# Performance work log

Hardware: AMD Instinct MI355X
Metric: run time of the kernel (lower is better)

The kernel has to match this reference:

```python
import jax, jax.numpy as jnp
import numpy as np

B, C_IN, C_OUT, N, E = 1, 64, 64, 100000, 3200000
BN_EPS = 1e-5


def setup_inputs() -> dict:
    key = jax.random.key(0)
    ks = jax.random.split(key, 8)
    return {
        "in_features": jax.random.normal(ks[0], (B, C_IN, N), dtype=jnp.float32),
        "w_v": jax.random.normal(ks[1], (C_OUT, C_IN), dtype=jnp.float32) * (1.0 / np.sqrt(C_IN)),
        "w_n": jax.random.normal(ks[2], (C_OUT, C_IN), dtype=jnp.float32) * (1.0 / np.sqrt(C_IN)),
        "gamma": jnp.ones((C_OUT,), dtype=jnp.float32),
        "beta": jnp.zeros((C_OUT,), dtype=jnp.float32),
        "prelu_a": jnp.full((1,), 0.25, dtype=jnp.float32),
        "reduce_index": jax.random.randint(ks[3], (E,), 0, N, dtype=jnp.int32),
        "gather_index": jax.random.randint(ks[4], (E,), 0, N, dtype=jnp.int32),
    }


def reference(in_features, w_v, w_n, gamma, beta, prelu_a, reduce_index, gather_index):
    # 1x1 convs == per-node linear maps: [B, C_in, N] -> [B, C_out, N]
    F_v = jnp.einsum('oi,bin->bon', w_v, in_features)
    F_n = jnp.einsum('oi,bin->bon', w_n, in_features)

    # gather source-node features per edge: [E, B, C_out]
    src = jnp.moveaxis(F_n[:, :, gather_index], 2, 0)
    # scatter-mean into destination nodes (include_self=False -> 0 for isolated nodes)
    sums = jax.ops.segment_sum(src, reduce_index, num_segments=N)  # [N, B, C]
    counts = jax.ops.segment_sum(jnp.ones((src.shape[0],), src.dtype), reduce_index,
                                 num_segments=N)  # [N]
    mean = sums / jnp.maximum(counts, 1.0)[:, None, None]  # nodes w/o edges stay 0
    out = jnp.moveaxis(mean, 0, 2) + F_v  # [B, C, N]

    # BatchNorm1d (training mode: biased batch stats over (B, N))
    mu = jnp.mean(out, axis=(0, 2), keepdims=True)
    var = jnp.mean((out - mu) ** 2, axis=(0, 2), keepdims=True)
    out = (out - mu) * jax.lax.rsqrt(var + BN_EPS)
    out = out * gamma[None, :, None] + beta[None, :, None]

    # PReLU with a single shared learnable slope
    out = jnp.where(out >= 0, out, prelu_a[0] * out)
    return out
```

## Files before the change

kernel.cpp:

```cpp
#include <hip/hip_runtime.h>
#include <hip/hip_bf16.h>

#define NODES 100000
#define BN_EPS 1e-5f
#define NB2 256
#define NPB2 391
#define CAP 13072
#define EPB 2048

__device__ __forceinline__ unsigned bf16rne(float f) {
    unsigned u = __float_as_uint(f);
    u += 0x7FFFu + ((u >> 16) & 1u);
    return u >> 16;
}
__device__ __forceinline__ float bflo(unsigned u) { return __uint_as_float(u << 16); }
__device__ __forceinline__ float bfhi(unsigned u) { return __uint_as_float(u & 0xFFFF0000u); }

__global__ __launch_bounds__(256, 8) void k_place(
        const int* __restrict__ ridx, const int* __restrict__ gidx,
        int* __restrict__ cursor, unsigned* __restrict__ packed, int E) {
    __shared__ int lh[4][NB2];
    const int t = threadIdx.x;
    const int w = t >> 6;
    for (int k = t; k < 4 * NB2; k += 256) ((int*)lh)[k] = 0;
    __syncthreads();
    const int base = blockIdx.x * EPB;
    int r[EPB / 256], g[EPB / 256];
#pragma unroll
    for (int k = 0; k < EPB / 256; ++k) {
        int e = base + t + (k << 8);
        r[k] = (e < E) ? ridx[e] : -1;
        g[k] = (e < E) ? gidx[e] : 0;
    }
#pragma unroll
    for (int k = 0; k < EPB / 256; ++k)
        if (r[k] >= 0) atomicAdd(&lh[w][(unsigned)r[k] / NPB2], 1);
    __syncthreads();
    {
        int c0 = lh[0][t], c1 = lh[1][t], c2 = lh[2][t], c3 = lh[3][t];
        int tot = c0 + c1 + c2 + c3;
        if (tot) {
            int g0 = t * CAP + atomicAdd(&cursor[t], tot);
            lh[0][t] = g0;
            lh[1][t] = g0 + c0;
            lh[2][t] = g0 + c0 + c1;
            lh[3][t] = g0 + c0 + c1 + c2;
        }
    }
    __syncthreads();
#pragma unroll
    for (int k = 0; k < EPB / 256; ++k) {
        if (r[k] >= 0) {
            unsigned rr = (unsigned)r[k];
            unsigned b = rr / NPB2;
            int off = atomicAdd(&lh[w][b], 1);
            if (off < (int)((b + 1) * CAP))
                packed[off] = ((rr - b * NPB2) << 17) | (unsigned)g[k];
        }
    }
}

__global__ __launch_bounds__(1024) void k_sortb(
        const int* __restrict__ cursor, unsigned* __restrict__ packed,
        int* __restrict__ nodestart, int* __restrict__ cnt) {
    __shared__ int lh[1024];
    __shared__ int lsc[1024];
    const int b = blockIdx.x, t = threadIdx.x;
    const int s0b = b * CAP;
    int cntb = cursor[b];
    if (cntb > CAP) cntb = CAP;
    unsigned r[(CAP + 1023) / 1024];
#pragma unroll
    for (int kk = 0; kk < (CAP + 1023) / 1024; ++kk) {
        int k = t + kk * 1024;
        if (k < cntb) r[kk] = packed[s0b + k];
    }
    lh[t] = 0;
    __syncthreads();
#pragma unroll
    for (int kk = 0; kk < (CAP + 1023) / 1024; ++kk) {
        int k = t + kk * 1024;
        if (k < cntb) atomicAdd(&lh[r[kk] >> 17], 1);
    }
    __syncthreads();
    lsc[t] = lh[t];
    __syncthreads();
    for (int off = 1; off < 1024; off <<= 1) {
        int v = lsc[t];
        int add = (t >= off) ? lsc[t - off] : 0;
        __syncthreads();
        lsc[t] = v + add;
        __syncthreads();
    }
    int excl = (t == 0) ? 0 : lsc[t - 1];
    if (t < NPB2) {
        int n = b * NPB2 + t;
        if (n < NODES) {
            nodestart[n] = s0b + excl;
            cnt[n] = lh[t];
        }
    }
    __syncthreads();
    lh[t] = excl;
    __syncthreads();
#pragma unroll
    for (int kk = 0; kk < (CAP + 1023) / 1024; ++kk) {
        int k = t + kk * 1024;
        if (k < cntb) {
            unsigned v = r[kk];
            int pos = atomicAdd(&lh[v >> 17], 1);
            packed[s0b + pos] = v & 0x1FFFFu;
        }
    }
}

__global__ __launch_bounds__(256, 4) void k_xpose(
        const float* __restrict__ x, unsigned* __restrict__ xb2) {
    __shared__ float lx[64 * 68];
    const int t = threadIdx.x;
    const int n0 = blockIdx.x * 64;
    for (int idx = t; idx < 1024; idx += 256) {
        int rr = idx >> 4;
        int q4 = (idx & 15) * 4;
        int n = n0 + q4;
        float4 xv = {0.f, 0.f, 0.f, 0.f};
        if (n < NODES) xv = *(const float4*)(x + (size_t)rr * NODES + n);
        *(float4*)&lx[rr * 68 + q4] = xv;
    }
    __syncthreads();
    const int c4 = (t & 15) * 4;
    const int j4 = (t >> 4) * 4;
    uint2* F2 = (uint2*)xb2;
#pragma unroll
    for (int k = 0; k < 4; ++k) {
        int n = n0 + j4 + k;
        if (n < NODES) {
            float v0 = lx[(c4 + 0) * 68 + j4 + k];
            float v1 = lx[(c4 + 1) * 68 + j4 + k];
            float v2 = lx[(c4 + 2) * 68 + j4 + k];
            float v3 = lx[(c4 + 3) * 68 + j4 + k];
            uint2 val;
            val.x = bf16rne(v0) | (bf16rne(v1) << 16);
            val.y = bf16rne(v2) | (bf16rne(v3) << 16);
            F2[n * 16 + (c4 >> 2)] = val;
        }
    }
}

__global__ __launch_bounds__(256) void k_gemm_n(
        const float* __restrict__ x, const float* __restrict__ wn,
        float* __restrict__ Fn) {
    __shared__ float lx[64][65];
    __shared__ float lw[64][65];
    const int t = threadIdx.x;
    const int n0 = blockIdx.x * 64;
    for (int idx = t; idx < 4096; idx += 256) {
        int r = idx >> 6, q = idx & 63;
        lw[r][q] = wn[idx];
        int n = n0 + q;
        lx[r][q] = (n < NODES) ? x[r * NODES + n] : 0.f;
    }
    __syncthreads();
    const int c = t & 63;
    const int jb = t >> 6;
    for (int k = 0; k < 16; ++k) {
        int j = jb + 4 * k;
        int n = n0 + j;
        if (n >= NODES) continue;
        float acc = 0.f;
#pragma unroll
        for (int ci = 0; ci < 64; ++ci)
            acc += lw[c][ci] * lx[ci][j];
        Fn[n * 64 + c] = acc;
    }
}

__global__ __launch_bounds__(256) void k_segreduce(
        const unsigned* __restrict__ Fnh2, const unsigned* __restrict__ packed,
        const int* __restrict__ nodestart, const int* __restrict__ cnt,
        float4* __restrict__ mean4) {
    const int n = (int)((blockIdx.x * 256u + threadIdx.x) >> 6);
    if (n >= NODES) return;
    const int lane = threadIdx.x & 63;
    const int sub = lane >> 3;
    const int cp  = lane & 7;
    const int s0 = nodestart[n];
    const int cn = cnt[n];
    const int s1 = s0 + cn;
    float f0 = 0.f, f1 = 0.f, f2 = 0.f, f3 = 0.f;
    float f4 = 0.f, f5 = 0.f, f6 = 0.f, f7 = 0.f;
    int i = s0;
    for (; i + 15 < s1; i += 16) {
        int ga = (int)packed[i + sub];
        int gb = (int)packed[i + 8 + sub];
        uint4 ua = *(const uint4*)(Fnh2 + (((size_t)ga) << 5) + (cp << 2));
        uint4 ub = *(const uint4*)(Fnh2 + (((size_t)gb) << 5) + (cp << 2));
        f0 += bflo(ua.x) + bflo(ub.x);
        f1 += bfhi(ua.x) + bfhi(ub.x);
        f2 += bflo(ua.y) + bflo(ub.y);
        f3 += bfhi(ua.y) + bfhi(ub.y);
        f4 += bflo(ua.z) + bflo(ub.z);
        f5 += bfhi(ua.z) + bfhi(ub.z);
        f6 += bflo(ua.w) + bflo(ub.w);
        f7 += bfhi(ua.w) + bfhi(ub.w);
    }
    for (; i < s1; i += 8) {
        uint4 u = {0u, 0u, 0u, 0u};
        if (i + sub < s1) {
            int g = (int)packed[i + sub];
            u = *(const uint4*)(Fnh2 + (((size_t)g) << 5) + (cp << 2));
        }
        f0 += bflo(u.x); f1 += bfhi(u.x);
        f2 += bflo(u.y); f3 += bfhi(u.y);
        f4 += bflo(u.z); f5 += bfhi(u.z);
        f6 += bflo(u.w); f7 += bfhi(u.w);
    }
#pragma unroll
    for (int m = 8; m < 64; m <<= 1) {
        f0 += __shfl_xor(f0, m);
        f1 += __shfl_xor(f1, m);
        f2 += __shfl_xor(f2, m);
        f3 += __shfl_xor(f3, m);
        f4 += __shfl_xor(f4, m);
        f5 += __shfl_xor(f5, m);
        f6 += __shfl_xor(f6, m);
        f7 += __shfl_xor(f7, m);
    }
    if (sub == 0) {
        float inv = 1.f / fmaxf((float)cn, 1.f);
        float4 lo4, hi4;
        lo4.x = f0 * inv; lo4.y = f1 * inv; lo4.z = f2 * inv; lo4.w = f3 * inv;
        hi4.x = f4 * inv; hi4.y = f5 * inv; hi4.z = f6 * inv; hi4.w = f7 * inv;
        mean4[n * 16 + cp * 2]     = lo4;
        mean4[n * 16 + cp * 2 + 1] = hi4;
    }
}

__global__ __launch_bounds__(256, 4) void k_combine128(
        const float* __restrict__ x, const float* __restrict__ wv,
        const float* __restrict__ wn, const float* __restrict__ meanx,
        float* __restrict__ outpre, float* __restrict__ bn) {
    __shared__ float lx[64 * 68];
    __shared__ float wt[64 * 68];
    __shared__ float reds[64][5];
    __shared__ float redq[64][5];
    const int t = threadIdx.x;
    const int n0 = blockIdx.x * 64;
    const int c4 = (t & 15) * 4;
    const int j4 = (t >> 4) * 4;
    for (int idx = t; idx < 1024; idx += 256) {
        int rr = idx >> 4;
        int q4 = (idx & 15) * 4;
        int n = n0 + q4;
        float4 xv = {0.f, 0.f, 0.f, 0.f};
        if (n < NODES) xv = *(const float4*)(x + (size_t)rr * NODES + n);
        *(float4*)&lx[rr * 68 + q4] = xv;
        float4 w4 = *(const float4*)(wv + (idx << 2));
        wt[(q4 + 0) * 68 + rr] = w4.x;
        wt[(q4 + 1) * 68 + rr] = w4.y;
        wt[(q4 + 2) * 68 + rr] = w4.z;
        wt[(q4 + 3) * 68 + rr] = w4.w;
    }
    __syncthreads();
    float4 a0 = {0,0,0,0}, a1 = {0,0,0,0}, a2 = {0,0,0,0}, a3 = {0,0,0,0};
#pragma unroll 8
    for (int ci = 0; ci < 64; ++ci) {
        float4 w = *(const float4*)&wt[ci * 68 + c4];
        float4 xv = *(const float4*)&lx[ci * 68 + j4];
        a0.x += w.x * xv.x; a0.y += w.x * xv.y; a0.z += w.x * xv.z; a0.w += w.x * xv.w;
        a1.x += w.y * xv.x; a1.y += w.y * xv.y; a1.z += w.y * xv.z; a1.w += w.y * xv.w;
        a2.x += w.z * xv.x; a2.y += w.z * xv.y; a2.z += w.z * xv.z; a2.w += w.z * xv.w;
        a3.x += w.w * xv.x; a3.y += w.w * xv.y; a3.z += w.w * xv.z; a3.w += w.w * xv.w;
    }
    __syncthreads();
    for (int idx = t; idx < 1024; idx += 256) {
        int j  = idx >> 4;
        int ci4 = (idx & 15) * 4;
        int n = n0 + j;
        float4 m4 = {0.f, 0.f, 0.f, 0.f};
        if (n < NODES) m4 = *(const float4*)(meanx + (size_t)n * 64 + ci4);
        lx[(ci4 + 0) * 68 + j] = m4.x;
        lx[(ci4 + 1) * 68 + j] = m4.y;
        lx[(ci4 + 2) * 68 + j] = m4.z;
        lx[(ci4 + 3) * 68 + j] = m4.w;
        int rr = idx >> 4;
        int q4 = (idx & 15) * 4;
        float4 w4 = *(const float4*)(wn + (idx << 2));
        wt[(q4 + 0) * 68 + rr] = w4.x;
        wt[(q4 + 1) * 68 + rr] = w4.y;
        wt[(q4 + 2) * 68 + rr] = w4.z;
        wt[(q4 + 3) * 68 + rr] = w4.w;
    }
    __syncthreads();
#pragma unroll 8
    for (int ci = 0; ci < 64; ++ci) {
        float4 w = *(const float4*)&wt[ci * 68 + c4];
        float4 xv = *(const float4*)&lx[ci * 68 + j4];
        a0.x += w.x * xv.x; a0.y += w.x * xv.y; a0.z += w.x * xv.z; a0.w += w.x * xv.w;
        a1.x += w.y * xv.x; a1.y += w.y * xv.y; a1.z += w.y * xv.z; a1.w += w.y * xv.w;
        a2.x += w.z * xv.x; a2.y += w.z * xv.y; a2.z += w.z * xv.z; a2.w += w.z * xv.w;
        a3.x += w.w * xv.x; a3.y += w.w * xv.y; a3.z += w.w * xv.z; a3.w += w.w * xv.w;
    }
    __syncthreads();
    float* tile = wt;
    float ls0 = 0.f, ls1 = 0.f, ls2 = 0.f, ls3 = 0.f;
    float lq0 = 0.f, lq1 = 0.f, lq2 = 0.f, lq3 = 0.f;
#pragma unroll
    for (int k = 0; k < 4; ++k) {
        int j = j4 + k;
        int n = n0 + j;
        float v0 = 0.f, v1 = 0.f, v2 = 0.f, v3 = 0.f;
        if (n < NODES) {
            v0 = (k == 0) ? a0.x : (k == 1) ? a0.y : (k == 2) ? a0.z : a0.w;
            v1 = (k == 0) ? a1.x : (k == 1) ? a1.y : (k == 2) ? a1.z : a1.w;
            v2 = (k == 0) ? a2.x : (k == 1) ? a2.y : (k == 2) ? a2.z : a2.w;
            v3 = (k == 0) ? a3.x : (k == 1) ? a3.y : (k == 2) ? a3.z : a3.w;
            ls0 += v0; lq0 += v0 * v0;
            ls1 += v1; lq1 += v1 * v1;
            ls2 += v2; lq2 += v2 * v2;
            ls3 += v3; lq3 += v3 * v3;
        }
        tile[(c4 + 0) * 65 + j] = v0;
        tile[(c4 + 1) * 65 + j] = v1;
        tile[(c4 + 2) * 65 + j] = v2;
        tile[(c4 + 3) * 65 + j] = v3;
    }
    const int lane = t & 63;
    const int wid = t >> 6;
#pragma unroll
    for (int m = 16; m < 64; m <<= 1) {
        ls0 += __shfl_xor(ls0, m); lq0 += __shfl_xor(lq0, m);
        ls1 += __shfl_xor(ls1, m); lq1 += __shfl_xor(lq1, m);
        ls2 += __shfl_xor(ls2, m); lq2 += __shfl_xor(lq2, m);
        ls3 += __shfl_xor(ls3, m); lq3 += __shfl_xor(lq3, m);
    }
    if (lane < 16) {
        reds[lane * 4 + 0][wid] = ls0; redq[lane * 4 + 0][wid] = lq0;
        reds[lane * 4 + 1][wid] = ls1; redq[lane * 4 + 1][wid] = lq1;
        reds[lane * 4 + 2][wid] = ls2; redq[lane * 4 + 2][wid] = lq2;
        reds[lane * 4 + 3][wid] = ls3; redq[lane * 4 + 3][wid] = lq3;
    }
    __syncthreads();
    const int j2 = t & 63;
    const int c2 = t >> 6;
    const int n = n0 + j2;
    if (n < NODES) {
        for (int k = 0; k < 16; ++k) {
            int cc = c2 + 4 * k;
            outpre[cc * NODES + n] = tile[cc * 65 + j2];
        }
    }
    if (t < 64) {
        float s = reds[t][0] + reds[t][1] + reds[t][2] + reds[t][3];
        float q = redq[t][0] + redq[t][1] + redq[t][2] + redq[t][3];
        atomicAdd(&bn[t], s);
        atomicAdd(&bn[64 + t], q);
    }
}

__global__ __launch_bounds__(256, 4) void k_combine_fb(
        const float* __restrict__ x, const float* __restrict__ wv,
        const float* __restrict__ sums, const int* __restrict__ counts,
        const int divide,
        float* __restrict__ outpre, float* __restrict__ bn) {
    __shared__ float lx[64 * 68];
    __shared__ float wt[64 * 68];
    __shared__ float reds[64][5];
    __shared__ float redq[64][5];
    const int t = threadIdx.x;
    const int n0 = blockIdx.x * 64;
    const int c4 = (t & 15) * 4;
    const int j4 = (t >> 4) * 4;
    float4 mv[4];
    const float4* sums4 = (const float4*)sums;
#pragma unroll
    for (int k = 0; k < 4; ++k) {
        int n = n0 + j4 + k;
        mv[k] = (n < NODES) ? sums4[n * 16 + (c4 >> 2)]
                            : float4{0.f, 0.f, 0.f, 0.f};
    }
    for (int idx = t; idx < 1024; idx += 256) {
        int rr = idx >> 4;
        int q4 = (idx & 15) * 4;
        int n = n0 + q4;
        float4 xv = {0.f, 0.f, 0.f, 0.f};
        if (n < NODES) xv = *(const float4*)(x + (size_t)rr * NODES + n);
        *(float4*)&lx[rr * 68 + q4] = xv;
        float4 w4 = *(const float4*)(wv + (idx << 2));
        wt[(q4 + 0) * 68 + rr] = w4.x;
        wt[(q4 + 1) * 68 + rr] = w4.y;
        wt[(q4 + 2) * 68 + rr] = w4.z;
        wt[(q4 + 3) * 68 + rr] = w4.w;
    }
    __syncthreads();
    float4 a0 = {0,0,0,0}, a1 = {0,0,0,0}, a2 = {0,0,0,0}, a3 = {0,0,0,0};
#pragma unroll 8
    for (int ci = 0; ci < 64; ++ci) {
        float4 w = *(const float4*)&wt[ci * 68 + c4];
        float4 xv = *(const float4*)&lx[ci * 68 + j4];
        a0.x += w.x * xv.x; a0.y += w.x * xv.y; a0.z += w.x * xv.z; a0.w += w.x * xv.w;
        a1.x += w.y * xv.x; a1.y += w.y * xv.y; a1.z += w.y * xv.z; a1.w += w.y * xv.w;
        a2.x += w.z * xv.x; a2.y += w.z * xv.y; a2.z += w.z * xv.z; a2.w += w.z * xv.w;
        a3.x += w.w * xv.x; a3.y += w.w * xv.y; a3.z += w.w * xv.z; a3.w += w.w * xv.w;
    }
    __syncthreads();
    float* tile = wt;
    float ls0 = 0.f, ls1 = 0.f, ls2 = 0.f, ls3 = 0.f;
    float lq0 = 0.f, lq1 = 0.f, lq2 = 0.f, lq3 = 0.f;
#pragma unroll
    for (int k = 0; k < 4; ++k) {
        int j = j4 + k;
        int n = n0 + j;
        float v0 = 0.f, v1 = 0.f, v2 = 0.f, v3 = 0.f;
        if (n < NODES) {
            float4 m = mv[k];
            if (divide) {
                float cf = fmaxf((float)counts[n], 1.f);
                m.x /= cf; m.y /= cf; m.z /= cf; m.w /= cf;
            }
            float b0 = (k == 0) ? a0.x : (k == 1) ? a0.y : (k == 2) ? a0.z : a0.w;
            float b1 = (k == 0) ? a1.x : (k == 1) ? a1.y : (k == 2) ? a1.z : a1.w;
            float b2 = (k == 0) ? a2.x : (k == 1) ? a2.y : (k == 2) ? a2.z : a2.w;
            float b3 = (k == 0) ? a3.x : (k == 1) ? a3.y : (k == 2) ? a3.z : a3.w;
            v0 = m.x + b0; v1 = m.y + b1; v2 = m.z + b2; v3 = m.w + b3;
            ls0 += v0; lq0 += v0 * v0;
            ls1 += v1; lq1 += v1 * v1;
            ls2 += v2; lq2 += v2 * v2;
            ls3 += v3; lq3 += v3 * v3;
        }
        tile[(c4 + 0) * 65 + j] = v0;
        tile[(c4 + 1) * 65 + j] = v1;
        tile[(c4 + 2) * 65 + j] = v2;
        tile[(c4 + 3) * 65 + j] = v3;
    }
    const int lane = t & 63;
    const int wid = t >> 6;
#pragma unroll
    for (int m = 16; m < 64; m <<= 1) {
        ls0 += __shfl_xor(ls0, m); lq0 += __shfl_xor(lq0, m);
        ls1 += __shfl_xor(ls1, m); lq1 += __shfl_xor(lq1, m);
        ls2 += __shfl_xor(ls2, m); lq2 += __shfl_xor(lq2, m);
        ls3 += __shfl_xor(ls3, m); lq3 += __shfl_xor(lq3, m);
    }
    if (lane < 16) {
        reds[lane * 4 + 0][wid] = ls0; redq[lane * 4 + 0][wid] = lq0;
        reds[lane * 4 + 1][wid] = ls1; redq[lane * 4 + 1][wid] = lq1;
        reds[lane * 4 + 2][wid] = ls2; redq[lane * 4 + 2][wid] = lq2;
        reds[lane * 4 + 3][wid] = ls3; redq[lane * 4 + 3][wid] = lq3;
    }
    __syncthreads();
    const int j2 = t & 63;
    const int c2 = t >> 6;
    const int n = n0 + j2;
    if (n < NODES) {
        for (int k = 0; k < 16; ++k) {
            int cc = c2 + 4 * k;
            outpre[cc * NODES + n] = tile[cc * 65 + j2];
        }
    }
    if (t < 64) {
        float s = reds[t][0] + reds[t][1] + reds[t][2] + reds[t][3];
        float q = redq[t][0] + redq[t][1] + redq[t][2] + redq[t][3];
        atomicAdd(&bn[t], s);
        atomicAdd(&bn[64 + t], q);
    }
}

__global__ __launch_bounds__(256) void k_final(
        float* __restrict__ out, const float* __restrict__ bn,
        const float* __restrict__ gamma, const float* __restrict__ beta,
        const float* __restrict__ pa) {
    const int c = blockIdx.y;
    const int n = blockIdx.x * 256 + threadIdx.x;
    const float invN = 1.f / (float)NODES;
    float mu = bn[c] * invN;
    float var = fmaxf(bn[64 + c] * invN - mu * mu, 0.f);
    float scale = gamma[c] * rsqrtf(var + BN_EPS);
    float shift = beta[c] - mu * scale;
    float a = pa[0];
    if (n < NODES) {
        float y = out[c * NODES + n] * scale + shift;
        y = (y >= 0.f) ? y : a * y;
        out[c * NODES + n] = y;
    }
}

__global__ __launch_bounds__(256) void k_scatter(
        const float* __restrict__ Fn,
        const int* __restrict__ gidx, const int* __restrict__ ridx,
        float* __restrict__ sums, int* __restrict__ counts, int E) {
    const int wave = (int)((blockIdx.x * blockDim.x + threadIdx.x) >> 6);
    const int lane = threadIdx.x & 63;
    const int base = wave * 64;
    if (base >= E) return;
    const int nvalid = min(64, E - base);
    int g = 0, r = 0;
    if (lane < nvalid) {
        g = gidx[base + lane];
        r = ridx[base + lane];
        atomicAdd(&counts[r], 1);
    }
    for (int i = 0; i < nvalid; ++i) {
        int gg = __shfl(g, i);
        int rr = __shfl(r, i);
        float v = Fn[gg * 64 + lane];
        atomicAdd(&sums[rr * 64 + lane], v);
    }
}

extern "C" void kernel_launch(void* const* d_in, const int* in_sizes, int n_in,
                              void* d_out, int out_size, void* d_ws, size_t ws_size,
                              hipStream_t stream) {
    const float* x     = (const float*)d_in[0];
    const float* w_v   = (const float*)d_in[1];
    const float* w_n   = (const float*)d_in[2];
    const float* gamma = (const float*)d_in[3];
    const float* beta  = (const float*)d_in[4];
    const float* pa    = (const float*)d_in[5];
    const int* ridx    = (const int*)d_in[6];
    const int* gidx    = (const int*)d_in[7];
    float* out = (float*)d_out;

    const int E = in_sizes[6];
    const long long N64 = (long long)NODES * 64;
    const int ntiles = (NODES + 63) / 64;
    const dim3 g4((NODES + 255) / 256, 64);

    size_t need = ((size_t)N64 + (size_t)NB2 * CAP + NB2 + 128
                   + NODES + NODES) * 4;

    if (ws_size >= need) {
        float*    meanx     = (float*)d_ws;
        unsigned* packed    = (unsigned*)(meanx + N64);
        int*      cursor    = (int*)(packed + (size_t)NB2 * CAP);
        float*    bn        = (float*)(cursor + NB2);
        int*      nodestart = (int*)(bn + 128);
        int*      cntarr    = nodestart + NODES;
        unsigned* xb = (unsigned*)out;

        hipMemsetAsync(cursor, 0, (NB2 + 128) * sizeof(int), stream);
        k_place<<<(E + EPB - 1) / EPB, 256, 0, stream>>>(ridx, gidx, cursor,
                                                         packed, E);
        k_xpose<<<ntiles, 256, 0, stream>>>(x, xb);
        k_sortb<<<NB2, 1024, 0, stream>>>(cursor, packed, nodestart, cntarr);
        k_segreduce<<<(NODES * 64 + 255) / 256, 256, 0, stream>>>(
            xb, packed, nodestart, cntarr, (float4*)meanx);
        k_combine128<<<ntiles, 256, 0, stream>>>(x, w_v, w_n, meanx, out, bn);
        k_final<<<g4, 256, 0, stream>>>(out, bn, gamma, beta, pa);
    } else {
        float* sums   = (float*)d_ws;
        int*   counts = (int*)(sums + N64);
        float* bn     = (float*)(sums + N64 + NODES);
        float* Fn = out;

        hipMemsetAsync(sums, 0, (size_t)(N64 + NODES + 128) * sizeof(float),
                       stream);
        k_gemm_n<<<ntiles, 256, 0, stream>>>(x, w_n, Fn);
        k_scatter<<<(E + 255) / 256, 256, 0, stream>>>(Fn, gidx, ridx, sums,
                                                       counts, E);
        k_combine_fb<<<ntiles, 256, 0, stream>>>(x, w_v, sums, counts, 1, out, bn);
        k_final<<<g4, 256, 0, stream>>>(out, bn, gamma, beta, pa);
    }
}
```

Baseline: 290.3 us.

## Replace bucketed two-pass edge sort with global histogram, scan, and atomic scatter CSR build

The two-level bucket sort (block-local placement into fixed-capacity buckets, then a per-bucket LDS sort) is replaced by a direct CSR build. A global per-node histogram is built with atomics, a two-kernel exclusive scan produces node offsets, and each edge is placed through a global atomic cursor. This removes the fixed per-bucket capacity and the LDS sorting pass, but relies on many scattered global atomics and random writes. The final BN/PReLU kernel is also vectorized to process four elements per thread with float4 loads and stores.

After: 657.6 us. 2.27x slower.

```diff
diff --git a/kernel.cpp b/kernel.cpp
--- a/kernel.cpp
+++ b/kernel.cpp
@@ -3,10 +3,8 @@
 
 #define NODES 100000
 #define BN_EPS 1e-5f
-#define NB2 256
-#define NPB2 391
-#define CAP 13072
-#define EPB 2048
+#define SBLK 1024
+#define NSB ((NODES + SBLK - 1) / SBLK)
 
 __device__ __forceinline__ unsigned bf16rne(float f) {
     unsigned u = __float_as_uint(f);
@@ -16,100 +14,93 @@
 __device__ __forceinline__ float bflo(unsigned u) { return __uint_as_float(u << 16); }
 __device__ __forceinline__ float bfhi(unsigned u) { return __uint_as_float(u & 0xFFFF0000u); }
 
-__global__ __launch_bounds__(256, 8) void k_place(
+__global__ __launch_bounds__(256) void k_hist(const int* __restrict__ ridx,
+                                              int* __restrict__ cnt, int E) {
+    int i4 = (blockIdx.x * 256 + threadIdx.x) * 4;
+    if (i4 + 3 < E) {
+        int4 r = *(const int4*)(ridx + i4);
+        atomicAdd(&cnt[r.x], 1);
+        atomicAdd(&cnt[r.y], 1);
+        atomicAdd(&cnt[r.z], 1);
+        atomicAdd(&cnt[r.w], 1);
+    } else {
+        for (int k = 0; k < 4; ++k)
+            if (i4 + k < E) atomicAdd(&cnt[ridx[i4 + k]], 1);
+    }
+}
+
+__global__ __launch_bounds__(SBLK) void k_scan1(
+        const int* __restrict__ cnt, int* __restrict__ nodestart,
+        int* __restrict__ bsum) {
+    __shared__ int lw[16];
+    const int t = threadIdx.x;
+    const int n = blockIdx.x * SBLK + t;
+    const int lane = t & 63;
+    const int wid = t >> 6;
+    int c = (n < NODES) ? cnt[n] : 0;
+    int v = c;
+#pragma unroll
+    for (int off = 1; off < 64; off <<= 1) {
+        int u = __shfl_up(v, off);
+        if (lane >= off) v += u;
+    }
+    if (lane == 63) lw[wid] = v;
+    __syncthreads();
+    if (t == 0) {
+        int s = 0;
+#pragma unroll
+        for (int i = 0; i < 16; ++i) { int x = lw[i]; lw[i] = s; s += x; }
+        bsum[blockIdx.x] = s;
+    }
+    __syncthreads();
+    if (n < NODES) nodestart[n] = v - c + lw[wid];
+}
+
+__global__ __launch_bounds__(SBLK) void k_scan2(
+        int* __restrict__ nodestart, int* __restrict__ cursor,
+        const int* __restrict__ bsum) {
+    __shared__ int partial[2];
+    __shared__ int soff;
+    const int t = threadIdx.x;
+    const int b = blockIdx.x;
+    if (t < 128) {
+        int v = (t < b) ? bsum[t] : 0;
+#pragma unroll
+        for (int m = 1; m < 64; m <<= 1) v += __shfl_xor(v, m);
+        if ((t & 63) == 0) partial[t >> 6] = v;
+    }
+    __syncthreads();
+    if (t == 0) soff = partial[0] + partial[1];
+    __syncthreads();
+    const int n = b * SBLK + t;
+    if (n < NODES) {
+        int ns = nodestart[n] + soff;
+        nodestart[n] = ns;
+        cursor[n] = ns;
+    }
+}
+
+__global__ __launch_bounds__(256) void k_scatter2(
         const int* __restrict__ ridx, const int* __restrict__ gidx,
         int* __restrict__ cursor, unsigned* __restrict__ packed, int E) {
-    __shared__ int lh[4][NB2];
-    const int t = threadIdx.x;
-    const int w = t >> 6;
-    for (int k = t; k < 4 * NB2; k += 256) ((int*)lh)[k] = 0;
-    __syncthreads();
-    const int base = blockIdx.x * EPB;
-    int r[EPB / 256], g[EPB / 256];
-#pragma unroll
-    for (int k = 0; k < EPB / 256; ++k) {
-        int e = base + t + (k << 8);
-        r[k] = (e < E) ? ridx[e] : -1;
-        g[k] = (e < E) ? gidx[e] : 0;
-    }
-#pragma unroll
-    for (int k = 0; k < EPB / 256; ++k)
-        if (r[k] >= 0) atomicAdd(&lh[w][(unsigned)r[k] / NPB2], 1);
-    __syncthreads();
-    {
-        int c0 = lh[0][t], c1 = lh[1][t], c2 = lh[2][t], c3 = lh[3][t];
-        int tot = c0 + c1 + c2 + c3;
-        if (tot) {
-            int g0 = t * CAP + atomicAdd(&cursor[t], tot);
-            lh[0][t] = g0;
-            lh[1][t] = g0 + c0;
-            lh[2][t] = g0 + c0 + c1;
-            lh[3][t] = g0 + c0 + c1 + c2;
-        }
-    }
-    __syncthreads();
-#pragma unroll
-    for (int k = 0; k < EPB / 256; ++k) {
-        if (r[k] >= 0) {
-            unsigned rr = (unsigned)r[k];
-            unsigned b = rr / NPB2;
-            int off = atomicAdd(&lh[w][b], 1);
-            if (off < (int)((b + 1) * CAP))
-                packed[off] = ((rr - b * NPB2) << 17) | (unsigned)g[k];
-        }
-    }
-}
-
-__global__ __launch_bounds__(1024) void k_sortb(
-        const int* __restrict__ cursor, unsigned* __restrict__ packed,
-        int* __restrict__ nodestart, int* __restrict__ cnt) {
-    __shared__ int lh[1024];
-    __shared__ int lsc[1024];
-    const int b = blockIdx.x, t = threadIdx.x;
-    const int s0b = b * CAP;
-    int cntb = cursor[b];
-    if (cntb > CAP) cntb = CAP;
-    unsigned r[(CAP + 1023) / 1024];
-#pragma unroll
-    for (int kk = 0; kk < (CAP + 1023) / 1024; ++kk) {
-        int k = t + kk * 1024;
-        if (k < cntb) r[kk] = packed[s0b + k];
-    }
-    lh[t] = 0;
-    __syncthreads();
-#pragma unroll
-    for (int kk = 0; kk < (CAP + 1023) / 1024; ++kk) {
-        int k = t + kk * 1024;
-        if (k < cntb) atomicAdd(&lh[r[kk] >> 17], 1);
-    }
-    __syncthreads();
-    lsc[t] = lh[t];
-    __syncthreads();
-    for (int off = 1; off < 1024; off <<= 1) {
-        int v = lsc[t];
-        int add = (t >= off) ? lsc[t - off] : 0;
-        __syncthreads();
-        lsc[t] = v + add;
-        __syncthreads();
-    }
-    int excl = (t == 0) ? 0 : lsc[t - 1];
-    if (t < NPB2) {
-        int n = b * NPB2 + t;
-        if (n < NODES) {
-            nodestart[n] = s0b + excl;
-            cnt[n] = lh[t];
-        }
-    }
-    __syncthreads();
-    lh[t] = excl;
-    __syncthreads();
-#pragma unroll
-    for (int kk = 0; kk < (CAP + 1023) / 1024; ++kk) {
-        int k = t + kk * 1024;
-        if (k < cntb) {
-            unsigned v = r[kk];
-            int pos = atomicAdd(&lh[v >> 17], 1);
-            packed[s0b + pos] = v & 0x1FFFFu;
+    int i4 = (blockIdx.x * 256 + threadIdx.x) * 4;
+    if (i4 + 3 < E) {
+        int4 r = *(const int4*)(ridx + i4);
+        int4 g = *(const int4*)(gidx + i4);
+        int p0 = atomicAdd(&cursor[r.x], 1);
+        int p1 = atomicAdd(&cursor[r.y], 1);
+        int p2 = atomicAdd(&cursor[r.z], 1);
+        int p3 = atomicAdd(&cursor[r.w], 1);
+        packed[p0] = (unsigned)g.x;
+        packed[p1] = (unsigned)g.y;
+        packed[p2] = (unsigned)g.z;
+        packed[p3] = (unsigned)g.w;
+    } else {
+        for (int k = 0; k < 4; ++k) {
+            if (i4 + k < E) {
+                int p = atomicAdd(&cursor[ridx[i4 + k]], 1);
+                packed[p] = (unsigned)gidx[i4 + k];
+            }
         }
     }
 }
@@ -471,17 +462,20 @@
         const float* __restrict__ gamma, const float* __restrict__ beta,
         const float* __restrict__ pa) {
     const int c = blockIdx.y;
-    const int n = blockIdx.x * 256 + threadIdx.x;
+    const int i4 = (blockIdx.x * 256 + threadIdx.x) * 4;
     const float invN = 1.f / (float)NODES;
     float mu = bn[c] * invN;
     float var = fmaxf(bn[64 + c] * invN - mu * mu, 0.f);
     float scale = gamma[c] * rsqrtf(var + BN_EPS);
     float shift = beta[c] - mu * scale;
     float a = pa[0];
-    if (n < NODES) {
-        float y = out[c * NODES + n] * scale + shift;
-        y = (y >= 0.f) ? y : a * y;
-        out[c * NODES + n] = y;
+    if (i4 < NODES) {
+        float4 y = *(float4*)(out + (size_t)c * NODES + i4);
+        y.x = y.x * scale + shift; y.x = (y.x >= 0.f) ? y.x : a * y.x;
+        y.y = y.y * scale + shift; y.y = (y.y >= 0.f) ? y.y : a * y.y;
+        y.z = y.z * scale + shift; y.z = (y.z >= 0.f) ? y.z : a * y.z;
+        y.w = y.w * scale + shift; y.w = (y.w >= 0.f) ? y.w : a * y.w;
+        *(float4*)(out + (size_t)c * NODES + i4) = y;
     }
 }
 
@@ -524,27 +518,29 @@
     const int E = in_sizes[6];
     const long long N64 = (long long)NODES * 64;
     const int ntiles = (NODES + 63) / 64;
-    const dim3 g4((NODES + 255) / 256, 64);
-
-    size_t need = ((size_t)N64 + (size_t)NB2 * CAP + NB2 + 128
-                   + NODES + NODES) * 4;
+    const dim3 g4((NODES / 4 + 255) / 256, 64);
+    const int eblk = (E + 1023) / 1024;
+
+    size_t need = ((size_t)N64 + (size_t)E + 3 * (size_t)NODES + 256) * 4;
 
     if (ws_size >= need) {
         float*    meanx     = (float*)d_ws;
         unsigned* packed    = (unsigned*)(meanx + N64);
-        int*      cursor    = (int*)(packed + (size_t)NB2 * CAP);
-        float*    bn        = (float*)(cursor + NB2);
+        int*      cnt       = (int*)(packed + E);
+        float*    bn        = (float*)(cnt + NODES);
         int*      nodestart = (int*)(bn + 128);
-        int*      cntarr    = nodestart + NODES;
+        int*      cursor    = nodestart + NODES;
+        int*      bsum      = cursor + NODES;
         unsigned* xb = (unsigned*)out;
 
-        hipMemsetAsync(cursor, 0, (NB2 + 128) * sizeof(int), stream);
-        k_place<<<(E + EPB - 1) / EPB, 256, 0, stream>>>(ridx, gidx, cursor,
-                                                         packed, E);
+        hipMemsetAsync(cnt, 0, (NODES + 128) * sizeof(int), stream);
+        k_hist<<<eblk, 256, 0, stream>>>(ridx, cnt, E);
         k_xpose<<<ntiles, 256, 0, stream>>>(x, xb);
-        k_sortb<<<NB2, 1024, 0, stream>>>(cursor, packed, nodestart, cntarr);
+        k_scan1<<<NSB, SBLK, 0, stream>>>(cnt, nodestart, bsum);
+        k_scan2<<<NSB, SBLK, 0, stream>>>(nodestart, cursor, bsum);
+        k_scatter2<<<eblk, 256, 0, stream>>>(ridx, gidx, cursor, packed, E);
         k_segreduce<<<(NODES * 64 + 255) / 256, 256, 0, stream>>>(
-            xb, packed, nodestart, cntarr, (float4*)meanx);
+            xb, packed, nodestart, cnt, (float4*)meanx);
         k_combine128<<<ntiles, 256, 0, stream>>>(x, w_v, w_n, meanx, out, bn);
         k_final<<<g4, 256, 0, stream>>>(out, bn, gamma, beta, pa);
     } else {
```
